# Optimization experiments

Measured on AMD Instinct MI355X. Metric: run time of the kernel, lower is better.

## Reference

```python
import jax, jax.numpy as jnp
import numpy as np

T, N, F = 12, 10000, 256
E = 160000
K = 3            # conv kernel size
NCONV = 3        # TCN layers
NLAYERS = 2      # GCN propagation layers per timestep
OUT = 64


def setup_inputs() -> dict:
    key = jax.random.key(0)
    ks = jax.random.split(key, 10)
    feats = jax.random.normal(ks[0], (T, N, F), dtype=jnp.float32)
    adjs = jax.random.randint(ks[1], (T, 2, E), 0, N)
    s = 1.0 / np.sqrt(F * K)
    conv_w = jax.random.uniform(ks[2], (NCONV, F, F, K), jnp.float32, -s, s)
    conv_b = jax.random.uniform(ks[3], (NCONV, F), jnp.float32, -s, s)
    gate_w = jax.random.uniform(ks[4], (NCONV, F, F, K), jnp.float32, -s, s)
    gate_b = jax.random.uniform(ks[5], (NCONV, F), jnp.float32, -s, s)
    sl = 1.0 / np.sqrt(F)
    lin_w = jax.random.uniform(ks[6], (OUT, F), jnp.float32, -sl, sl)
    lin_b = jax.random.uniform(ks[7], (OUT,), jnp.float32, -sl, sl)
    return {"feats": feats, "adjs": adjs, "conv_w": conv_w, "conv_b": conv_b,
            "gate_w": gate_w, "gate_b": gate_b, "lin_w": lin_w, "lin_b": lin_b}


def _ax(x, edge_index):
    # sparse A @ X: gather source node features, scatter-sum at target nodes
    src, dst = edge_index[0], edge_index[1]
    return jax.ops.segment_sum(x[src], dst, num_segments=x.shape[0])


def _causal_conv(x, w, b):
    # x: [N, C, T]; causal left pad then VALID conv
    xp = jnp.pad(x, ((0, 0), (0, 0), (K - 1, 0)))
    y = jax.lax.conv_general_dilated(xp, w, (1,), 'VALID',
                                     dimension_numbers=('NCH', 'OIH', 'NCH'))
    return y + b[None, :, None]


def reference(feats, adjs, conv_w, conv_b, gate_w, gate_b, lin_w, lin_b):
    x = feats  # [T, N, F]
    for _ in range(NLAYERS):
        x = jax.vmap(_ax)(x, adjs)
    emb = jnp.transpose(x, (1, 2, 0))  # [N, F, T]
    for i in range(NCONV):
        c = _causal_conv(emb, conv_w[i], conv_b[i])
        g = _causal_conv(emb, gate_w[i], gate_b[i])
        emb = c * jax.nn.sigmoid(g)
    out = emb[:, :, -1] @ lin_w.T + lin_b  # [N, OUT]
    return jax.nn.log_softmax(out, axis=1)
```

## Files before the change

### kernel.cpp

```cpp
#include <hip/hip_runtime.h>
#include <cstdint>
#include <cstddef>

#define T_DIM   12
#define N_NODES 10000
#define F_DIM   256
#define E_EDGES 160000
#define NSLOT   7
#define OUT_DIM 64
#define CG_BM   128

typedef _Float16 f16;
typedef _Float16 f16x8 __attribute__((ext_vector_type(8)));
typedef _Float16 f16x4 __attribute__((ext_vector_type(4)));
typedef float    f32x4 __attribute__((ext_vector_type(4)));

typedef __attribute__((address_space(1))) const void* as1_cvp;
typedef __attribute__((address_space(3))) void*       as3_vp;

__device__ __forceinline__ void glds16(const void* g, void* l) {
    __builtin_amdgcn_global_load_lds((as1_cvp)g, (as3_vp)l, 16, 0, 0);
}

__global__ __launch_bounds__(256) void zero_i32_kernel(int* __restrict__ p, int n) {
    int i = blockIdx.x * 256 + threadIdx.x;
    if (i < n) p[i] = 0;
}

__global__ __launch_bounds__(256) void feats2f16_kernel(const float* __restrict__ feats,
                                                        f16* __restrict__ xout) {
    int idx = blockIdx.x * 256 + threadIdx.x;
    const int total = NSLOT * N_NODES * F_DIM;
    int i0 = idx * 8;
    if (i0 >= total) return;
    const float* src = feats + (size_t)5 * N_NODES * F_DIM + i0;
    float4 a = *(const float4*)src;
    float4 b = *(const float4*)(src + 4);
    f16x8 o;
    o[0] = (f16)a.x; o[1] = (f16)a.y; o[2] = (f16)a.z; o[3] = (f16)a.w;
    o[4] = (f16)b.x; o[5] = (f16)b.y; o[6] = (f16)b.z; o[7] = (f16)b.w;
    *(f16x8*)(xout + i0) = o;
}

__global__ __launch_bounds__(256) void count_kernel(const int* __restrict__ adjs,
                                                    int* __restrict__ counts) {
    int idx = blockIdx.x * 256 + threadIdx.x;
    if (idx >= NSLOT * E_EDGES) return;
    int s = idx / E_EDGES;
    int e = idx - s * E_EDGES;
    int dst = adjs[(size_t)(5 + s) * 2 * E_EDGES + E_EDGES + e];
    atomicAdd(&counts[s * N_NODES + dst], 1);
}

__global__ __launch_bounds__(1024) void scan_kernel(const int* __restrict__ counts,
                                                    int* __restrict__ offsets) {
    int s = blockIdx.x, tid = threadIdx.x;
    const int* c = counts + s * N_NODES;
    int* o = offsets + s * (N_NODES + 1);
    __shared__ int wsum[16];
    int vals[10];
    int tsum = 0;
    int base = tid * 10;
    #pragma unroll
    for (int j = 0; j < 10; ++j) {
        int i = base + j;
        int v = (i < N_NODES) ? c[i] : 0;
        vals[j] = tsum;
        tsum += v;
    }
    int lane = tid & 63, wid = tid >> 6;
    int x = tsum;
    #pragma unroll
    for (int d = 1; d < 64; d <<= 1) { int y = __shfl_up(x, d); if (lane >= d) x += y; }
    if (lane == 63) wsum[wid] = x;
    __syncthreads();
    if (wid == 0 && lane < 16) {
        int wv = wsum[lane];
        #pragma unroll
        for (int d = 1; d < 16; d <<= 1) { int y = __shfl_up(wv, d); if (lane >= d) wv += y; }
        wsum[lane] = wv;
    }
    __syncthreads();
    int waveoff = (wid == 0) ? 0 : wsum[wid - 1];
    int ex = waveoff + (x - tsum);
    #pragma unroll
    for (int j = 0; j < 10; ++j) {
        int i = base + j;
        if (i < N_NODES) o[i] = ex + vals[j];
    }
    if (tid == 1023) o[N_NODES] = wsum[15];
}

__global__ __launch_bounds__(256) void fill_kernel(const int* __restrict__ adjs,
                                                   const int* __restrict__ offsets,
                                                   int* __restrict__ cursor,
                                                   int* __restrict__ esrc) {
    int idx = blockIdx.x * 256 + threadIdx.x;
    if (idx >= NSLOT * E_EDGES) return;
    int s = idx / E_EDGES;
    int e = idx - s * E_EDGES;
    const int* a = adjs + (size_t)(5 + s) * 2 * E_EDGES;
    int src = a[e];
    int dst = a[E_EDGES + e];
    int pos = atomicAdd(&cursor[s * N_NODES + dst], 1);
    esrc[(size_t)s * E_EDGES + offsets[s * (N_NODES + 1) + dst] + pos] = src;
}

__global__ __launch_bounds__(256) void ax16_kernel(const f16* __restrict__ xin,
                                                   f16* __restrict__ xout,
                                                   const int* __restrict__ offsets,
                                                   const int* __restrict__ esrc) {
    int s = blockIdx.x & 7;
    if (s >= NSLOT) return;
    int n = ((blockIdx.x >> 3) << 2) + (threadIdx.x >> 6);
    int lane = threadIdx.x & 63;
    const int* off = offsets + s * (N_NODES + 1);
    int j0 = off[n], j1 = off[n + 1];
    const f16* base = xin + (size_t)s * N_NODES * F_DIM + lane * 4;
    const int* es = esrc + (size_t)s * E_EDGES;
    float ax = 0.f, ay = 0.f, az = 0.f, aw = 0.f;
    int j = j0;
    for (; j + 8 <= j1; j += 8) {
        int i0 = es[j], i1 = es[j+1], i2 = es[j+2], i3 = es[j+3];
        int i4 = es[j+4], i5 = es[j+5], i6 = es[j+6], i7 = es[j+7];
        f16x4 r0 = *(const f16x4*)(base + (size_t)i0 * F_DIM);
        f16x4 r1 = *(const f16x4*)(base + (size_t)i1 * F_DIM);
        f16x4 r2 = *(const f16x4*)(base + (size_t)i2 * F_DIM);
        f16x4 r3 = *(const f16x4*)(base + (size_t)i3 * F_DIM);
        f16x4 r4 = *(const f16x4*)(base + (size_t)i4 * F_DIM);
        f16x4 r5 = *(const f16x4*)(base + (size_t)i5 * F_DIM);
        f16x4 r6 = *(const f16x4*)(base + (size_t)i6 * F_DIM);
        f16x4 r7 = *(const f16x4*)(base + (size_t)i7 * F_DIM);
        ax += (((float)r0[0] + (float)r1[0]) + ((float)r2[0] + (float)r3[0]))
            + (((float)r4[0] + (float)r5[0]) + ((float)r6[0] + (float)r7[0]));
        ay += (((float)r0[1] + (float)r1[1]) + ((float)r2[1] + (float)r3[1]))
            + (((float)r4[1] + (float)r5[1]) + ((float)r6[1] + (float)r7[1]));
        az += (((float)r0[2] + (float)r1[2]) + ((float)r2[2] + (float)r3[2]))
            + (((float)r4[2] + (float)r5[2]) + ((float)r6[2] + (float)r7[2]));
        aw += (((float)r0[3] + (float)r1[3]) + ((float)r2[3] + (float)r3[3]))
            + (((float)r4[3] + (float)r5[3]) + ((float)r6[3] + (float)r7[3]));
    }
    for (; j < j1; ++j) {
        f16x4 r = *(const f16x4*)(base + (size_t)es[j] * F_DIM);
        ax += (float)r[0]; ay += (float)r[1]; az += (float)r[2]; aw += (float)r[3];
    }
    f16x4 o;
    o[0] = (f16)ax; o[1] = (f16)ay; o[2] = (f16)az; o[3] = (f16)aw;
    *(f16x4*)(xout + ((size_t)s * N_NODES + n) * F_DIM + lane * 4) = o;
}

__global__ __launch_bounds__(256) void wtrans16_kernel(const float* __restrict__ cw,
                                                       const float* __restrict__ gw,
                                                       f16* __restrict__ wTt) {
    int idx = blockIdx.x * 256 + threadIdx.x;
    if (idx >= 3 * 4 * 24 * 2 * 64 * 32) return;
    int k   = idx & 31;
    int col = (idx >> 5) & 63;
    int cg  = (idx >> 11) & 1;
    int r   = idx >> 12;
    int lbo = r / 24;
    int kk  = r - lbo * 24;
    int l   = lbo >> 2, bo = lbo & 3;
    int K   = kk * 32 + k;
    int tap = K >> 8;
    int ci  = K & 255;
    int o   = bo * 64 + col;
    const float* src = cg ? gw : cw;
    wTt[idx] = (f16)src[(((size_t)l * 256 + o) * 256 + ci) * 3 + tap];
}

__global__ __launch_bounds__(256) void conv_gemm_f16_kernel(
    const f16* __restrict__ xin, f16* __restrict__ xout,
    const f16* __restrict__ wTt,
    const float* __restrict__ biasc, const float* __restrict__ biasg,
    int M, int in_slot_base, int out_slot0)
{
    __shared__ __align__(16) f16 lds[8192];

    const int tid = threadIdx.x;
    const int ln  = tid & 63;
    const int w   = __builtin_amdgcn_readfirstlane(tid >> 6);
    const int bm  = blockIdx.x, bo = blockIdx.y;
    const int wr  = w >> 1, wc = w & 1;

    const size_t SLOTB = (size_t)N_NODES * F_DIM * 2;
    const char* xin_b = (const char*)xin + (size_t)in_slot_base * SLOTB;
    int r0  = 32 * w + (ln >> 2);
    int gr0 = bm * CG_BM + r0;      if (gr0 > M - 1) gr0 = M - 1;
    int gr1 = bm * CG_BM + r0 + 16; if (gr1 > M - 1) gr1 = M - 1;
    int sg0 = gr0 / N_NODES, nn0 = gr0 - sg0 * N_NODES;
    int sg1 = gr1 / N_NODES, nn1 = gr1 - sg1 * N_NODES;
    const char* aptr0 = xin_b + (size_t)sg0 * SLOTB + (size_t)nn0 * 512 + (ln & 3) * 16;
    const char* aptr1 = xin_b + (size_t)sg1 * SLOTB + (size_t)nn1 * 512 + (ln & 3) * 16;
    const char* bptr  = (const char*)wTt + (size_t)bo * (24 * 8192)
                        + (size_t)(2 * w) * 1024 + (size_t)ln * 16;

    f16* ldsA0 = &lds[(2 * w    ) * 512];
    f16* ldsA1 = &lds[(2 * w + 1) * 512];
    f16* ldsB0 = &lds[4096 + (2 * w    ) * 512];
    f16* ldsB1 = &lds[4096 + (2 * w + 1) * 512];

    const int aoff = (wr * 64 + (ln & 15)) * 32 + (ln >> 4) * 8;
    const int boff = 4096 + (wc * 32 + (ln & 15)) * 32 + (ln >> 4) * 8;

    f32x4 acc_c[4][2] = {};
    f32x4 acc_g[4][2] = {};

    for (int kk = 0; kk < 24; ++kk) {
        const size_t aoffb = (size_t)(kk >> 3) * SLOTB + (size_t)(kk & 7) * 64;
        const char* gb = bptr + (size_t)kk * 8192;
        glds16(aptr0 + aoffb, ldsA0);
        glds16(aptr1 + aoffb, ldsA1);
        glds16(gb,        ldsB0);
        glds16(gb + 1024, ldsB1);
        __syncthreads();

        f16x8 af0 = *(const f16x8*)&lds[aoff];
        f16x8 af1 = *(const f16x8*)&lds[aoff + 512];
        f16x8 af2 = *(const f16x8*)&lds[aoff + 1024];
        f16x8 af3 = *(const f16x8*)&lds[aoff + 1536];
        f16x8 bc0 = *(const f16x8*)&lds[boff];
        f16x8 bc1 = *(const f16x8*)&lds[boff + 512];
        f16x8 bg0 = *(const f16x8*)&lds[boff + 2048];
        f16x8 bg1 = *(const f16x8*)&lds[boff + 2560];

        acc_c[0][0] = __builtin_amdgcn_mfma_f32_16x16x32_f16(af0, bc0, acc_c[0][0], 0, 0, 0);
        acc_g[0][0] = __builtin_amdgcn_mfma_f32_16x16x32_f16(af0, bg0, acc_g[0][0], 0, 0, 0);
        acc_c[0][1] = __builtin_amdgcn_mfma_f32_16x16x32_f16(af0, bc1, acc_c[0][1], 0, 0, 0);
        acc_g[0][1] = __builtin_amdgcn_mfma_f32_16x16x32_f16(af0, bg1, acc_g[0][1], 0, 0, 0);
        acc_c[1][0] = __builtin_amdgcn_mfma_f32_16x16x32_f16(af1, bc0, acc_c[1][0], 0, 0, 0);
        acc_g[1][0] = __builtin_amdgcn_mfma_f32_16x16x32_f16(af1, bg0, acc_g[1][0], 0, 0, 0);
        acc_c[1][1] = __builtin_amdgcn_mfma_f32_16x16x32_f16(af1, bc1, acc_c[1][1], 0, 0, 0);
        acc_g[1][1] = __builtin_amdgcn_mfma_f32_16x16x32_f16(af1, bg1, acc_g[1][1], 0, 0, 0);
        acc_c[2][0] = __builtin_amdgcn_mfma_f32_16x16x32_f16(af2, bc0, acc_c[2][0], 0, 0, 0);
        acc_g[2][0] = __builtin_amdgcn_mfma_f32_16x16x32_f16(af2, bg0, acc_g[2][0], 0, 0, 0);
        acc_c[2][1] = __builtin_amdgcn_mfma_f32_16x16x32_f16(af2, bc1, acc_c[2][1], 0, 0, 0);
        acc_g[2][1] = __builtin_amdgcn_mfma_f32_16x16x32_f16(af2, bg1, acc_g[2][1], 0, 0, 0);
        acc_c[3][0] = __builtin_amdgcn_mfma_f32_16x16x32_f16(af3, bc0, acc_c[3][0], 0, 0, 0);
        acc_g[3][0] = __builtin_amdgcn_mfma_f32_16x16x32_f16(af3, bg0, acc_g[3][0], 0, 0, 0);
        acc_c[3][1] = __builtin_amdgcn_mfma_f32_16x16x32_f16(af3, bc1, acc_c[3][1], 0, 0, 0);
        acc_g[3][1] = __builtin_amdgcn_mfma_f32_16x16x32_f16(af3, bg1, acc_g[3][1], 0, 0, 0);

        __syncthreads();
    }

    #pragma unroll
    for (int rb = 0; rb < 4; ++rb) {
        int grow0 = bm * CG_BM + wr * 64 + rb * 16 + ((ln >> 4) << 2);
        #pragma unroll
        for (int cf = 0; cf < 2; ++cf) {
            int gcol = bo * 64 + wc * 32 + cf * 16 + (ln & 15);
            float bc = biasc[gcol], bg = biasg[gcol];
            #pragma unroll
            for (int r = 0; r < 4; ++r) {
                int grow = grow0 + r;
                if (grow < M) {
                    int sg = grow / N_NODES;
                    int nn = grow - sg * N_NODES;
                    float cv = acc_c[rb][cf][r] + bc;
                    float gv = acc_g[rb][cf][r] + bg;
                    float y  = cv / (1.0f + expf(-gv));
                    xout[((size_t)(out_slot0 + sg) * N_NODES + nn) * F_DIM + gcol] = (f16)y;
                }
            }
        }
    }
}

__global__ __launch_bounds__(64) void head_kernel(const f16* __restrict__ emb,
                                                  const float* __restrict__ lin_w,
                                                  const float* __restrict__ lin_b,
                                                  float* __restrict__ out) {
    int n = blockIdx.x;
    int tid = threadIdx.x;
    __shared__ float row[F_DIM];
    f16x4 hv = *(const f16x4*)(emb + (size_t)n * F_DIM + tid * 4);
    row[tid * 4 + 0] = (float)hv[0];
    row[tid * 4 + 1] = (float)hv[1];
    row[tid * 4 + 2] = (float)hv[2];
    row[tid * 4 + 3] = (float)hv[3];
    __syncthreads();
    float acc = lin_b[tid];
    const float* w = lin_w + (size_t)tid * F_DIM;
    #pragma unroll 8
    for (int c = 0; c < F_DIM; c += 4) {
        float4 wv = *(const float4*)(w + c);
        acc += row[c] * wv.x + row[c + 1] * wv.y + row[c + 2] * wv.z + row[c + 3] * wv.w;
    }
    float mx = acc;
    #pragma unroll
    for (int s = 32; s > 0; s >>= 1) mx = fmaxf(mx, __shfl_xor(mx, s));
    float ex = expf(acc - mx);
    float sum = ex;
    #pragma unroll
    for (int s = 32; s > 0; s >>= 1) sum += __shfl_xor(sum, s);
    out[(size_t)n * OUT_DIM + tid] = acc - mx - logf(sum);
}

extern "C" void kernel_launch(void* const* d_in, const int* in_sizes, int n_in,
                              void* d_out, int out_size, void* d_ws, size_t ws_size,
                              hipStream_t stream) {
    (void)in_sizes; (void)n_in; (void)out_size; (void)ws_size;
    const float* feats  = (const float*)d_in[0];
    const int*   adjs   = (const int*)d_in[1];
    const float* conv_w = (const float*)d_in[2];
    const float* conv_b = (const float*)d_in[3];
    const float* gate_w = (const float*)d_in[4];
    const float* gate_b = (const float*)d_in[5];
    const float* lin_w  = (const float*)d_in[6];
    const float* lin_b  = (const float*)d_in[7];
    float* out = (float*)d_out;

    char* ws = (char*)d_ws;
    const size_t SX16 = (size_t)NSLOT * N_NODES * F_DIM * 2;
    const size_t OXF  = 0;
    const size_t OXP  = OXF + SX16;
    const size_t OXA  = OXP + SX16;
    const size_t OXB  = OXA + SX16;
    const size_t OWT  = OXB + SX16;
    const size_t OCN  = OWT + 2359296;
    const size_t OOF  = OCN + 280000;
    const size_t OES  = OOF + 280064;

    f16*   x16f    = (f16*)  (ws + OXF);
    f16*   x16p    = (f16*)  (ws + OXP);
    f16*   x16a    = (f16*)  (ws + OXA);
    f16*   x16b    = (f16*)  (ws + OXB);
    f16*   wTt     = (f16*)  (ws + OWT);
    int*   counts  = (int*)  (ws + OCN);
    int*   offsets = (int*)  (ws + OOF);
    int*   esrc    = (int*)  (ws + OES);

    const int ncnt = NSLOT * N_NODES;
    const int nedge_thr = NSLOT * E_EDGES;
    const int LWT = 4 * 24 * 2 * 64 * 32;
    const int nconv8 = NSLOT * N_NODES * F_DIM / 8;

    zero_i32_kernel<<<(ncnt + 255) / 256, 256, 0, stream>>>(counts, ncnt);
    count_kernel<<<(nedge_thr + 255) / 256, 256, 0, stream>>>(adjs, counts);
    scan_kernel<<<NSLOT, 1024, 0, stream>>>(counts, offsets);
    zero_i32_kernel<<<(ncnt + 255) / 256, 256, 0, stream>>>(counts, ncnt);
    fill_kernel<<<(nedge_thr + 255) / 256, 256, 0, stream>>>(adjs, offsets, counts, esrc);

    wtrans16_kernel<<<(3 * LWT + 255) / 256, 256, 0, stream>>>(conv_w, gate_w, wTt);
    feats2f16_kernel<<<(nconv8 + 255) / 256, 256, 0, stream>>>(feats, x16f);

    ax16_kernel<<<8 * (N_NODES / 4), 256, 0, stream>>>(x16f, x16p, offsets, esrc);
    ax16_kernel<<<8 * (N_NODES / 4), 256, 0, stream>>>(x16p, x16a, offsets, esrc);

    const int M0 = 5 * N_NODES;
    conv_gemm_f16_kernel<<<dim3((M0 + CG_BM - 1) / CG_BM, 4), 256, 0, stream>>>(
        x16a, x16b, wTt, conv_b, gate_b, M0, 0, 2);
    const int M1 = 3 * N_NODES;
    conv_gemm_f16_kernel<<<dim3((M1 + CG_BM - 1) / CG_BM, 4), 256, 0, stream>>>(
        x16b, x16a, wTt + LWT, conv_b + 256, gate_b + 256, M1, 2, 4);
    const int M2 = 1 * N_NODES;
    conv_gemm_f16_kernel<<<dim3((M2 + CG_BM - 1) / CG_BM, 4), 256, 0, stream>>>(
        x16a, x16b, wTt + 2 * LWT, conv_b + 512, gate_b + 512, M2, 4, 6);

    head_kernel<<<N_NODES, 64, 0, stream>>>(x16b + (size_t)6 * N_NODES * F_DIM, lin_w, lin_b, out);
}
```

Measured before the change: 659.6 us.

## Triple-buffer LDS in conv GEMM with two-stage-ahead async prefetch

The gated conv GEMM previously loaded each K-slice into a single LDS buffer and waited for it before computing, leaving the global-to-LDS load latency exposed. It now uses three LDS buffers and issues loads two iterations ahead, using explicit vmcnt waits and raw barriers so loads for later slices overlap the MFMAs of the current one. This triples LDS use per block, which can lower occupancy. The hand-written waitcnt and barrier ordering has to stay correct for the async loads.

New measurement: 628.1 us. -4.8%, faster.

```diff
diff --git a/kernel.cpp b/kernel.cpp
--- a/kernel.cpp
+++ b/kernel.cpp
@@ -175,7 +175,7 @@
     const float* __restrict__ biasc, const float* __restrict__ biasg,
     int M, int in_slot_base, int out_slot0)
 {
-    __shared__ __align__(16) f16 lds[8192];
+    __shared__ __align__(16) f16 lds[3 * 8192];
 
     const int tid = threadIdx.x;
     const int ln  = tid & 63;
@@ -195,34 +195,47 @@
     const char* bptr  = (const char*)wTt + (size_t)bo * (24 * 8192)
                         + (size_t)(2 * w) * 1024 + (size_t)ln * 16;
 
-    f16* ldsA0 = &lds[(2 * w    ) * 512];
-    f16* ldsA1 = &lds[(2 * w + 1) * 512];
-    f16* ldsB0 = &lds[4096 + (2 * w    ) * 512];
-    f16* ldsB1 = &lds[4096 + (2 * w + 1) * 512];
-
     const int aoff = (wr * 64 + (ln & 15)) * 32 + (ln >> 4) * 8;
     const int boff = 4096 + (wc * 32 + (ln & 15)) * 32 + (ln >> 4) * 8;
 
     f32x4 acc_c[4][2] = {};
     f32x4 acc_g[4][2] = {};
 
-    for (int kk = 0; kk < 24; ++kk) {
+    auto STAGE = [&](int kk, int p) {
         const size_t aoffb = (size_t)(kk >> 3) * SLOTB + (size_t)(kk & 7) * 64;
         const char* gb = bptr + (size_t)kk * 8192;
-        glds16(aptr0 + aoffb, ldsA0);
-        glds16(aptr1 + aoffb, ldsA1);
-        glds16(gb,        ldsB0);
-        glds16(gb + 1024, ldsB1);
-        __syncthreads();
-
-        f16x8 af0 = *(const f16x8*)&lds[aoff];
-        f16x8 af1 = *(const f16x8*)&lds[aoff + 512];
-        f16x8 af2 = *(const f16x8*)&lds[aoff + 1024];
-        f16x8 af3 = *(const f16x8*)&lds[aoff + 1536];
-        f16x8 bc0 = *(const f16x8*)&lds[boff];
-        f16x8 bc1 = *(const f16x8*)&lds[boff + 512];
-        f16x8 bg0 = *(const f16x8*)&lds[boff + 2048];
-        f16x8 bg1 = *(const f16x8*)&lds[boff + 2560];
+        f16* base = lds + p * 8192;
+        glds16(aptr0 + aoffb, base + (2 * w    ) * 512);
+        glds16(aptr1 + aoffb, base + (2 * w + 1) * 512);
+        glds16(gb,        base + 4096 + (2 * w    ) * 512);
+        glds16(gb + 1024, base + 4096 + (2 * w + 1) * 512);
+    };
+
+    STAGE(0, 0);
+    STAGE(1, 1);
+
+    #pragma unroll
+    for (int kk = 0; kk < 24; ++kk) {
+        const int p = kk % 3;
+        if (kk < 22) {
+            STAGE(kk + 2, (kk + 2) % 3);
+            asm volatile("s_waitcnt vmcnt(8)" ::: "memory");
+        } else if (kk == 22) {
+            asm volatile("s_waitcnt vmcnt(4)" ::: "memory");
+        } else {
+            asm volatile("s_waitcnt vmcnt(0)" ::: "memory");
+        }
+        __builtin_amdgcn_s_barrier();
+
+        const f16* L = lds + p * 8192;
+        f16x8 af0 = *(const f16x8*)&L[aoff];
+        f16x8 af1 = *(const f16x8*)&L[aoff + 512];
+        f16x8 af2 = *(const f16x8*)&L[aoff + 1024];
+        f16x8 af3 = *(const f16x8*)&L[aoff + 1536];
+        f16x8 bc0 = *(const f16x8*)&L[boff];
+        f16x8 bc1 = *(const f16x8*)&L[boff + 512];
+        f16x8 bg0 = *(const f16x8*)&L[boff + 2048];
+        f16x8 bg1 = *(const f16x8*)&L[boff + 2560];
 
         acc_c[0][0] = __builtin_amdgcn_mfma_f32_16x16x32_f16(af0, bc0, acc_c[0][0], 0, 0, 0);
         acc_g[0][0] = __builtin_amdgcn_mfma_f32_16x16x32_f16(af0, bg0, acc_g[0][0], 0, 0, 0);
@@ -241,8 +254,9 @@
         acc_c[3][1] = __builtin_amdgcn_mfma_f32_16x16x32_f16(af3, bc1, acc_c[3][1], 0, 0, 0);
         acc_g[3][1] = __builtin_amdgcn_mfma_f32_16x16x32_f16(af3, bg1, acc_g[3][1], 0, 0, 0);
 
-        __syncthreads();
-    }
+        __builtin_amdgcn_s_barrier();
+    }
+    __builtin_amdgcn_sched_barrier(0);
 
     #pragma unroll
     for (int rb = 0; rb < 4; ++rb) {
```
